# Performance work log

Hardware: AMD Instinct MI355X
Metric: run time of the kernel (lower is better)

## Reference

```python
import jax, jax.numpy as jnp
import numpy as np

DIM = 2048
N_HEADS = 16
HEAD_DIM = 128

def setup_inputs() -> dict:
    key = jax.random.key(0)
    ks = jax.random.split(key, 7)
    B, S = 4, 2048
    x = jax.random.normal(ks[0], (B, S, DIM), dtype=jnp.float32)
    cos = jax.random.uniform(ks[1], (S, HEAD_DIM // 2), dtype=jnp.float32)
    sin = jax.random.uniform(ks[2], (S, HEAD_DIM // 2), dtype=jnp.float32)
    scale = 1.0 / np.sqrt(DIM)
    wq = jax.random.normal(ks[3], (DIM, N_HEADS * HEAD_DIM), dtype=jnp.float32) * scale
    wk = jax.random.normal(ks[4], (DIM, N_HEADS * HEAD_DIM), dtype=jnp.float32) * scale
    wv = jax.random.normal(ks[5], (DIM, N_HEADS * HEAD_DIM), dtype=jnp.float32) * scale
    wo = jax.random.normal(ks[6], (N_HEADS * HEAD_DIM, DIM), dtype=jnp.float32) * scale
    return {"x": x, "cos": cos, "sin": sin, "wq": wq, "wk": wk, "wv": wv, "wo": wo}

def _apply_rope(x, cos, sin):
    # x: [B, H, S, D]; cos/sin: [S, D//2]
    d = x.shape[-1] // 2
    x1, x2 = x[..., :d], x[..., d:]
    c = cos[None, None, :x.shape[2], :d]
    s = sin[None, None, :x.shape[2], :d]
    return jnp.concatenate([x1 * c - x2 * s, x2 * c + x1 * s], axis=-1)

def reference(x, cos, sin, wq, wk, wv, wo):
    B, S, _ = x.shape
    q = (x @ wq).reshape(B, S, N_HEADS, HEAD_DIM).transpose(0, 2, 1, 3)
    k = (x @ wk).reshape(B, S, N_HEADS, HEAD_DIM).transpose(0, 2, 1, 3)
    v = (x @ wv).reshape(B, S, N_HEADS, HEAD_DIM).transpose(0, 2, 1, 3)
    q = _apply_rope(q, cos, sin)
    k = _apply_rope(k, cos, sin)
    scale = 1.0 / jnp.sqrt(jnp.asarray(HEAD_DIM, dtype=x.dtype))
    scores = jnp.einsum('bhqd,bhkd->bhqk', q, k) * scale  # [B,H,S,S]
    causal = jnp.tril(jnp.ones((S, S), dtype=bool))
    scores = jnp.where(causal[None, None], scores, jnp.asarray(-jnp.inf, dtype=scores.dtype))
    attn = jax.nn.softmax(scores, axis=-1)
    out = jnp.einsum('bhqk,bhkd->bhqd', attn, v)
    out = out.transpose(0, 2, 1, 3).reshape(B, S, N_HEADS * HEAD_DIM)
    return out @ wo
```

## Files before the change

### kernel.cpp

```cpp
#include <hip/hip_runtime.h>
#include <cstdint>
#include <cstddef>

#define DIM 2048
#define NHEADS 16
#define HD 128
#define BATCH 4
#define SEQ 2048
#define MROWS (BATCH*SEQ)
#define NT 32
#define TSZ (256*64)

typedef __attribute__((ext_vector_type(4))) float  f32x4;
typedef __attribute__((ext_vector_type(4))) float  float4v;
typedef __attribute__((ext_vector_type(8))) short  short8;
typedef __attribute__((ext_vector_type(4))) short  short4v;
typedef __attribute__((ext_vector_type(4))) unsigned uint4v;
typedef __attribute__((ext_vector_type(8))) __bf16 bf16x8;

#define QSCALE 0.1275173772f

__device__ __forceinline__ unsigned f2bfbits(float f) {
  unsigned u = __builtin_bit_cast(unsigned, f);
  return (u + 0x7FFFu + ((u >> 16) & 1u)) >> 16;
}
__device__ __forceinline__ short f2bf(float f) { return (short)f2bfbits(f); }
__device__ __forceinline__ float bf2f(short s) {
  unsigned u = ((unsigned)(unsigned short)s) << 16;
  return __builtin_bit_cast(float, u);
}
__device__ __forceinline__ unsigned cvtpk_bf16(float lo, float hi) {
  unsigned r;
  asm("v_cvt_pk_bf16_f32 %0, %1, %2" : "=v"(r) : "v"(lo), "v"(hi));
  return r;
}
__device__ __forceinline__ f32x4 mfma16(short8 a, short8 b, f32x4 c) {
  return __builtin_amdgcn_mfma_f32_16x16x32_bf16(
      __builtin_bit_cast(bf16x8, a), __builtin_bit_cast(bf16x8, b), c, 0, 0, 0);
}
__device__ __forceinline__ void gload16(const short* g, short* l) {
  __builtin_amdgcn_global_load_lds(
      (const __attribute__((address_space(1))) unsigned int*)g,
      (__attribute__((address_space(3))) unsigned int*)l, 16, 0, 0);
}

__global__ __launch_bounds__(256) void k_convert_x(const float* __restrict__ x,
                                                   short* __restrict__ xb) {
  size_t i = ((size_t)blockIdx.x * 256 + threadIdx.x) * 8;
  float4v a = *(const float4v*)(x + i);
  float4v b = *(const float4v*)(x + i + 4);
  short8 o;
  o[0] = f2bf(a[0]); o[1] = f2bf(a[1]); o[2] = f2bf(a[2]); o[3] = f2bf(a[3]);
  o[4] = f2bf(b[0]); o[5] = f2bf(b[1]); o[6] = f2bf(b[2]); o[7] = f2bf(b[3]);
  *(short8*)(xb + i) = o;
}

__global__ __launch_bounds__(256) void k_transpose_w(
    const float* __restrict__ w0, const float* __restrict__ w1,
    const float* __restrict__ w2, const float* __restrict__ w3,
    short* __restrict__ o0, short* __restrict__ o1,
    short* __restrict__ o2, short* __restrict__ o3) {
  const float* w; short* o;
  switch (blockIdx.z) {
    case 0: w = w0; o = o0; break;
    case 1: w = w1; o = o1; break;
    case 2: w = w2; o = o2; break;
    default: w = w3; o = o3; break;
  }
  __shared__ float tile[32][33];
  int tx = threadIdx.x, ty = threadIdx.y;
  int kb = blockIdx.y * 32, nb = blockIdx.x * 32;
#pragma unroll
  for (int i = 0; i < 4; ++i)
    tile[ty + 8 * i][tx] = w[(size_t)(kb + ty + 8 * i) * DIM + nb + tx];
  __syncthreads();
#pragma unroll
  for (int i = 0; i < 4; ++i)
    o[(size_t)(nb + ty + 8 * i) * DIM + kb + tx] = f2bf(tile[tx][ty + 8 * i]);
}

template<int MODE>
__global__ __launch_bounds__(512, 2) void k_gemm256(const short* __restrict__ A,
                                                    const short* __restrict__ BtAll,
                                                    const float* __restrict__ cosg,
                                                    const float* __restrict__ sing,
                                                    short* __restrict__ Qp,
                                                    short* __restrict__ Kp,
                                                    short* __restrict__ Vp,
                                                    float* __restrict__ Of) {
  __shared__ short As[2 * TSZ];
  __shared__ short Bs[2 * TSZ];
  const int t = threadIdx.x;
  const int lane = t & 63, wid = t >> 6;
  const int wm = wid >> 2, wn = wid & 3;
  const int gi = lane >> 4, li = lane & 15;
  const int stg = (wid ^ (wid >> 2)) & 1;
  const int id = blockIdx.x;
  const int wg = MODE == 0 ? ((id & 7) * 96 + (id >> 3)) : ((id & 7) * 32 + (id >> 3));
  const int bm = wg & 31, bn = wg >> 5;
  const int m0 = bm * 256;
  const int which = MODE == 0 ? (bn >> 3) : 0;
  const int n0 = MODE == 0 ? ((bn & 7) * 256) : (bn * 256);
  const short* Bg = BtAll + (size_t)which * DIM * DIM;
  const short* Ag = A;

  const int lrow = lane >> 3;
  const int lcol = ((lane & 7) ^ lrow) * 8;
  const int hh = wn >> 1, hf = wn & 1;

  auto bcol = [&](int j) {
    if (MODE == 0) return hh * 128 + (j >> 1) * 64 + hf * 32 + (j & 1) * 16;
    return wn * 64 + j * 16;
  };

  f32x4 acc[8][4];
#pragma unroll
  for (int i = 0; i < 8; ++i)
#pragma unroll
    for (int j = 0; j < 4; ++j) acc[i][j] = (f32x4){0.f, 0.f, 0.f, 0.f};

#define STAGE_TILE(tt, buf)                                                       \
  {                                                                               \
    const int kk0 = (tt) * 64;                                                    \
    short* asd = As + (buf) * TSZ;                                                \
    short* bsd = Bs + (buf) * TSZ;                                                \
    _Pragma("unroll")                                                             \
    for (int ii = 0; ii < 4; ++ii) {                                              \
      int rb = ii * 64 + wid * 8;                                                 \
      gload16(Ag + (size_t)(m0 + rb + lrow) * DIM + kk0 + lcol, asd + rb * 64);   \
      gload16(Bg + (size_t)(n0 + rb + lrow) * DIM + kk0 + lcol, bsd + rb * 64);   \
    }                                                                             \
  }

  STAGE_TILE(0, 0)
  STAGE_TILE(1, 1)

  for (int tt = 0; tt < NT; ++tt) {
    if (tt < NT - 1) asm volatile("s_waitcnt vmcnt(8)" ::: "memory");
    else             asm volatile("s_waitcnt vmcnt(0)" ::: "memory");
    __builtin_amdgcn_s_barrier();
    const short* Asb = As + (tt & 1) * TSZ;
    const short* Bsb = Bs + (tt & 1) * TSZ;

#pragma unroll 1
    for (int ph = 0; ph < 2; ++ph) {
      const int ks = ph ^ stg;
      short8 av[8], bv[4];
      const int sw = (((ks << 2) | gi) ^ (li & 7)) * 8;
#pragma unroll
      for (int i = 0; i < 8; ++i)
        av[i] = *(const short8*)&Asb[(wm * 128 + i * 16 + li) * 64 + sw];
#pragma unroll
      for (int j = 0; j < 4; ++j)
        bv[j] = *(const short8*)&Bsb[(bcol(j) + li) * 64 + sw];
      __builtin_amdgcn_s_setprio(1);
#pragma unroll
      for (int i = 0; i < 8; ++i)
#pragma unroll
        for (int j = 0; j < 4; ++j)
          acc[i][j] = mfma16(av[i], bv[j], acc[i][j]);
      __builtin_amdgcn_s_setprio(0);
    }
    __builtin_amdgcn_s_barrier();
    if (tt + 2 < NT) STAGE_TILE(tt + 2, tt & 1)
  }
#undef STAGE_TILE

  if (MODE == 1) {
#pragma unroll
    for (int i = 0; i < 8; ++i)
#pragma unroll
      for (int j = 0; j < 4; ++j)
#pragma unroll
        for (int r = 0; r < 4; ++r) {
          int gm = m0 + wm * 128 + i * 16 + gi * 4 + r;
          int gn = n0 + wn * 64 + j * 16 + li;
          Of[(size_t)gm * DIM + gn] = acc[i][j][r];
        }
    return;
  }
  const int h = 2 * (bn & 7) + hh;
  if (which == 2) {
#pragma unroll
    for (int i = 0; i < 8; ++i)
#pragma unroll
      for (int j = 0; j < 4; ++j) {
        int gm0 = m0 + wm * 128 + i * 16 + gi * 4;
        int b = gm0 >> 11, s0 = gm0 & 2047;
        int d = (j >> 1) * 64 + hf * 32 + (j & 1) * 16 + li;
        short4v pk;
#pragma unroll
        for (int r = 0; r < 4; ++r) pk[r] = f2bf(acc[i][j][r]);
        *(short4v*)&Vp[((size_t)(b * NHEADS + h) * HD + d) * SEQ + s0] = pk;
      }
  } else {
    short* O = which ? Kp : Qp;
    const float qs = which ? 1.0f : QSCALE;
#pragma unroll
    for (int i = 0; i < 8; ++i)
#pragma unroll
      for (int j = 0; j < 2; ++j) {
        int dlo = hf * 32 + j * 16 + li;
#pragma unroll
        for (int r = 0; r < 4; ++r) {
          int gm = m0 + wm * 128 + i * 16 + gi * 4 + r;
          int b = gm >> 11, s = gm & 2047;
          float c = cosg[s * 64 + dlo], sn = sing[s * 64 + dlo];
          float a = acc[i][j][r], bb = acc[i][j + 2][r];
          size_t base = ((size_t)(b * NHEADS + h) * SEQ + s) * HD;
          O[base + dlo]      = f2bf((a * c - bb * sn) * qs);
          O[base + dlo + 64] = f2bf((bb * c + a * sn) * qs);
        }
      }
  }
}

__global__ __launch_bounds__(512) void k_flash(const short* __restrict__ Qg,
                                               const short* __restrict__ Kg,
                                               const short* __restrict__ Vg,
                                               short* __restrict__ Og) {
  __shared__ short Kl[2 * 64 * 128];
  __shared__ short Vl[2 * 128 * 64];
  const int t = threadIdx.x, lane = t & 63, wid = t >> 6;
  const int gi = lane >> 4, li = lane & 15;
  const int id = blockIdx.x;
  const int ip = 15 - (id >> 6);
  const int bh = id & 63;
  const int q0 = ip * 128;
  const short* Qb = Qg + (size_t)bh * SEQ * HD;
  const short* Kb = Kg + (size_t)bh * SEQ * HD;
  const short* Vb = Vg + (size_t)bh * HD * SEQ;
  const int mrow = q0 + wid * 16 + li;
  const int nt = 2 * ip + 2;

  short8 qb[4];
#pragma unroll
  for (int kk = 0; kk < 4; ++kk)
    qb[kk] = *(const short8*)(Qb + (size_t)mrow * HD + kk * 32 + 8 * gi);

  f32x4 o[8];
#pragma unroll
  for (int d = 0; d < 8; ++d) o[d] = (f32x4){0.f, 0.f, 0.f, 0.f};
  float mx = -1e30f, lsum = 0.f;
  const int srcA = li | ((lane & 16) << 1);
  const int srcB = srcA + 16;
  const bool hig = (lane & 32) != 0;

#define FSTAGE(tt, buf)                                                           \
  {                                                                               \
    const int kk0 = (tt) * 64;                                                    \
    short* kl = Kl + (buf) * 8192;                                                \
    short* vl = Vl + (buf) * 8192;                                                \
    _Pragma("unroll")                                                             \
    for (int u = 0; u < 2; ++u) {                                                 \
      int w = wid * 2 + u;                                                        \
      { int row = w * 4 + (lane >> 4); int sl = (lane & 15) ^ (row & 15);         \
        gload16(Kb + (size_t)(kk0 + row) * HD + sl * 8, kl + w * 512); }          \
      { int row = w * 8 + (lane >> 3); int sl = (lane & 7) ^ (row & 7);           \
        gload16(Vb + (size_t)row * SEQ + kk0 + sl * 8, vl + w * 512); }           \
    }                                                                             \
  }

  FSTAGE(0, 0)

  for (int tt = 0; tt < nt; ++tt) {
    const int k0 = tt * 64;
    if (tt + 1 < nt) {
      FSTAGE(tt + 1, (tt + 1) & 1)
      asm volatile("s_waitcnt vmcnt(4)" ::: "memory");
    } else {
      asm volatile("s_waitcnt vmcnt(0)" ::: "memory");
    }
    __builtin_amdgcn_s_barrier();
    const short* Kc = Kl + (tt & 1) * 8192;
    const short* Vc = Vl + (tt & 1) * 8192;

    f32x4 sacc[4];
#pragma unroll
    for (int af = 0; af < 4; ++af) sacc[af] = (f32x4){0.f, 0.f, 0.f, 0.f};
    __builtin_amdgcn_s_setprio(1);
#pragma unroll
    for (int kk = 0; kk < 4; ++kk)
#pragma unroll
      for (int af = 0; af < 4; ++af) {
        short8 kf = *(const short8*)&Kc[(16 * af + li) * 128 + (((kk << 2) | gi) ^ li) * 8];
        sacc[af] = mfma16(kf, qb[kk], sacc[af]);
      }
    __builtin_amdgcn_s_setprio(0);

    float p[4][4];
    float pmax = -1e30f;
    const bool mask = (k0 + 63 > mrow);
#pragma unroll
    for (int af = 0; af < 4; ++af)
#pragma unroll
      for (int r = 0; r < 4; ++r) {
        float v = sacc[af][r];
        if (mask && (k0 + 16 * af + 4 * gi + r > mrow)) v = -1e30f;
        p[af][r] = v;
        pmax = fmaxf(pmax, v);
      }
    pmax = fmaxf(pmax, __shfl_xor(pmax, 16));
    pmax = fmaxf(pmax, __shfl_xor(pmax, 32));
    if (!__all(pmax <= mx + 11.54f)) {
      float mnew = fmaxf(mx, pmax);
      float alpha = __builtin_amdgcn_exp2f(mx - mnew);
      lsum *= alpha;
      mx = mnew;
#pragma unroll
      for (int d = 0; d < 8; ++d) o[d] *= alpha;
    }
    float psum = 0.f;
#pragma unroll
    for (int af = 0; af < 4; ++af)
#pragma unroll
      for (int r = 0; r < 4; ++r) {
        float e = __builtin_amdgcn_exp2f(p[af][r] - mx);
        p[af][r] = e;
        psum += e;
      }
    psum += __shfl_xor(psum, 16);
    psum += __shfl_xor(psum, 32);
    lsum += psum;

    unsigned plo[4], phi[4];
#pragma unroll
    for (int af = 0; af < 4; ++af) {
      plo[af] = cvtpk_bf16(p[af][0], p[af][1]);
      phi[af] = cvtpk_bf16(p[af][2], p[af][3]);
    }
#pragma unroll
    for (int kk2 = 0; kk2 < 2; ++kk2) {
      unsigned aAlo = (unsigned)__shfl((int)plo[2 * kk2], srcA);
      unsigned aAhi = (unsigned)__shfl((int)phi[2 * kk2], srcA);
      unsigned aBlo = (unsigned)__shfl((int)plo[2 * kk2 + 1], srcA);
      unsigned aBhi = (unsigned)__shfl((int)phi[2 * kk2 + 1], srcA);
      unsigned bAlo = (unsigned)__shfl((int)plo[2 * kk2], srcB);
      unsigned bAhi = (unsigned)__shfl((int)phi[2 * kk2], srcB);
      unsigned bBlo = (unsigned)__shfl((int)plo[2 * kk2 + 1], srcB);
      unsigned bBhi = (unsigned)__shfl((int)phi[2 * kk2 + 1], srcB);
      uint4v dws;
      dws[0] = hig ? aBlo : aAlo;
      dws[1] = hig ? aBhi : aAhi;
      dws[2] = hig ? bBlo : bAlo;
      dws[3] = hig ? bBhi : bAhi;
      short8 pbf = __builtin_bit_cast(short8, dws);
      __builtin_amdgcn_s_setprio(1);
#pragma unroll
      for (int d = 0; d < 8; ++d) {
        short8 vf = *(const short8*)&Vc[(16 * d + li) * 64 + ((((kk2 << 2) | gi)) ^ (li & 7)) * 8];
        o[d] = mfma16(vf, pbf, o[d]);
      }
      __builtin_amdgcn_s_setprio(0);
    }
    __builtin_amdgcn_s_barrier();
  }
#undef FSTAGE

  const float inv = 1.0f / lsum;
  const int b = bh >> 4, h = bh & 15;
  const size_t obase = ((size_t)b * SEQ + mrow) * DIM + h * HD;
#pragma unroll
  for (int d = 0; d < 8; ++d) {
    short4v st;
#pragma unroll
    for (int r = 0; r < 4; ++r) st[r] = f2bf(o[d][r] * inv);
    *(short4v*)&Og[obase + d * 16 + 4 * gi] = st;
  }
}

extern "C" void kernel_launch(void* const* d_in, const int* in_sizes, int n_in,
                              void* d_out, int out_size, void* d_ws, size_t ws_size,
                              hipStream_t stream) {
  (void)in_sizes; (void)n_in; (void)out_size;
  const float* x    = (const float*)d_in[0];
  const float* cosg = (const float*)d_in[1];
  const float* sing = (const float*)d_in[2];
  const float* wq   = (const float*)d_in[3];
  const float* wk   = (const float*)d_in[4];
  const float* wv   = (const float*)d_in[5];
  const float* wo   = (const float*)d_in[6];

  const size_t SZ = (size_t)MROWS * DIM * 2;
  char* ws = (char*)d_ws;
  short* xb  = (short*)ws;
  short* wqT = (short*)(ws + SZ);
  short* wkT = wqT + (size_t)DIM * DIM;
  short* wvT = wkT + (size_t)DIM * DIM;
  short* woT = wvT + (size_t)DIM * DIM;
  short *Qp, *Kp, *Vp;
  if (ws_size >= 5 * SZ) {
    Qp = (short*)(ws + 2 * SZ);
    Kp = (short*)(ws + 3 * SZ);
    Vp = (short*)(ws + 4 * SZ);
  } else {
    Qp = (short*)d_out;
    Kp = (short*)d_out + SZ / 2;
    Vp = (short*)(ws + 2 * SZ);
  }
  short* Ob = xb;

  k_convert_x<<<8192, 256, 0, stream>>>(x, xb);
  k_transpose_w<<<dim3(64, 64, 4), dim3(32, 8), 0, stream>>>(wq, wk, wv, wo,
                                                             wqT, wkT, wvT, woT);
  k_gemm256<0><<<768, 512, 0, stream>>>(xb, wqT, cosg, sing, Qp, Kp, Vp, nullptr);
  k_flash<<<1024, 512, 0, stream>>>(Qp, Kp, Vp, Ob);
  k_gemm256<1><<<256, 512, 0, stream>>>(Ob, woT, nullptr, nullptr,
                                        nullptr, nullptr, nullptr, (float*)d_out);
}
```

Measured before the change: 434.7 us.

## Interleave half-tile global loads with MFMA phases in the 256x256 GEMM

```diff
diff --git a/kernel.cpp b/kernel.cpp
--- a/kernel.cpp
+++ b/kernel.cpp
@@ -80,7 +80,7 @@
 }
 
 template<int MODE>
-__global__ __launch_bounds__(512, 2) void k_gemm256(const short* __restrict__ A,
+__global__ __launch_bounds__(512, 1) void k_gemm256(const short* __restrict__ A,
                                                     const short* __restrict__ BtAll,
                                                     const float* __restrict__ cosg,
                                                     const float* __restrict__ sing,
@@ -94,7 +94,6 @@
   const int lane = t & 63, wid = t >> 6;
   const int wm = wid >> 2, wn = wid & 3;
   const int gi = lane >> 4, li = lane & 15;
-  const int stg = (wid ^ (wid >> 2)) & 1;
   const int id = blockIdx.x;
   const int wg = MODE == 0 ? ((id & 7) * 96 + (id >> 3)) : ((id & 7) * 32 + (id >> 3));
   const int bm = wg & 31, bn = wg >> 5;
@@ -113,58 +112,89 @@
     return wn * 64 + j * 16;
   };
 
+  auto stageA = [&](int h, int tile) {
+    const int kk0 = tile * 64;
+    short* d = As + (tile & 1) * TSZ;
+#pragma unroll
+    for (int u = 0; u < 2; ++u) {
+      int rb = h * 128 + u * 64 + wid * 8;
+      gload16(Ag + (size_t)(m0 + rb + lrow) * DIM + kk0 + lcol, d + rb * 64);
+    }
+  };
+  auto stageB = [&](int h, int tile) {
+    const int kk0 = tile * 64;
+    short* d = Bs + (tile & 1) * TSZ;
+#pragma unroll
+    for (int u = 0; u < 2; ++u) {
+      int rb = h * 128 + u * 64 + wid * 8;
+      gload16(Bg + (size_t)(n0 + rb + lrow) * DIM + kk0 + lcol, d + rb * 64);
+    }
+  };
+
   f32x4 acc[8][4];
 #pragma unroll
   for (int i = 0; i < 8; ++i)
 #pragma unroll
     for (int j = 0; j < 4; ++j) acc[i][j] = (f32x4){0.f, 0.f, 0.f, 0.f};
 
-#define STAGE_TILE(tt, buf)                                                       \
-  {                                                                               \
-    const int kk0 = (tt) * 64;                                                    \
-    short* asd = As + (buf) * TSZ;                                                \
-    short* bsd = Bs + (buf) * TSZ;                                                \
+#define READ_AV(IH, KS)                                                           \
+  { const int sw = ((((KS) << 2) | gi) ^ (li & 7)) * 8;                           \
     _Pragma("unroll")                                                             \
-    for (int ii = 0; ii < 4; ++ii) {                                              \
-      int rb = ii * 64 + wid * 8;                                                 \
-      gload16(Ag + (size_t)(m0 + rb + lrow) * DIM + kk0 + lcol, asd + rb * 64);   \
-      gload16(Bg + (size_t)(n0 + rb + lrow) * DIM + kk0 + lcol, bsd + rb * 64);   \
-    }                                                                             \
-  }
-
-  STAGE_TILE(0, 0)
-  STAGE_TILE(1, 1)
+    for (int i = 0; i < 4; ++i)                                                   \
+      av[i] = *(const short8*)&Ab[(wm * 128 + ((IH) * 4 + i) * 16 + li) * 64 + sw]; }
+#define READ_BV(DST, KS)                                                          \
+  { const int sw = ((((KS) << 2) | gi) ^ (li & 7)) * 8;                           \
+    _Pragma("unroll")                                                             \
+    for (int j = 0; j < 4; ++j)                                                   \
+      DST[j] = *(const short8*)&Bb[(bcol(j) + li) * 64 + sw]; }
+#define PHASE_MFMA(IH, BV)                                                        \
+  __builtin_amdgcn_s_barrier();                                                   \
+  __builtin_amdgcn_s_setprio(1);                                                  \
+  _Pragma("unroll")                                                               \
+  for (int i = 0; i < 4; ++i)                                                     \
+    _Pragma("unroll")                                                             \
+    for (int j = 0; j < 4; ++j)                                                   \
+      acc[(IH) * 4 + i][j] = mfma16(av[i], BV[j], acc[(IH) * 4 + i][j]);          \
+  __builtin_amdgcn_s_setprio(0);
+
+  stageB(0, 0); stageB(1, 0);
+  stageA(0, 0); stageA(1, 0);
+  stageB(0, 1); stageB(1, 1);
+  asm volatile("s_waitcnt vmcnt(4)" ::: "memory");
+  __builtin_amdgcn_s_barrier();
 
   for (int tt = 0; tt < NT; ++tt) {
-    if (tt < NT - 1) asm volatile("s_waitcnt vmcnt(8)" ::: "memory");
+    const short* Ab = As + (tt & 1) * TSZ;
+    const short* Bb = Bs + (tt & 1) * TSZ;
+    short8 av[4], bv0[4], bv1[4];
+
+    READ_AV(0, 0)
+    READ_BV(bv0, 0)
+    if (tt + 1 < NT) stageA(0, tt + 1);
+    PHASE_MFMA(0, bv0)
+    __builtin_amdgcn_s_barrier();
+
+    READ_AV(0, 1)
+    READ_BV(bv1, 1)
+    if (tt + 1 < NT) stageA(1, tt + 1);
+    PHASE_MFMA(0, bv1)
+    __builtin_amdgcn_s_barrier();
+
+    READ_AV(1, 0)
+    if (tt + 2 < NT) stageB(0, tt + 2);
+    PHASE_MFMA(1, bv0)
+    __builtin_amdgcn_s_barrier();
+
+    READ_AV(1, 1)
+    if (tt + 2 < NT) stageB(1, tt + 2);
+    PHASE_MFMA(1, bv1)
+    if (tt + 2 < NT) asm volatile("s_waitcnt vmcnt(4)" ::: "memory");
     else             asm volatile("s_waitcnt vmcnt(0)" ::: "memory");
     __builtin_amdgcn_s_barrier();
-    const short* Asb = As + (tt & 1) * TSZ;
-    const short* Bsb = Bs + (tt & 1) * TSZ;
-
-#pragma unroll 1
-    for (int ph = 0; ph < 2; ++ph) {
-      const int ks = ph ^ stg;
-      short8 av[8], bv[4];
-      const int sw = (((ks << 2) | gi) ^ (li & 7)) * 8;
-#pragma unroll
-      for (int i = 0; i < 8; ++i)
-        av[i] = *(const short8*)&Asb[(wm * 128 + i * 16 + li) * 64 + sw];
-#pragma unroll
-      for (int j = 0; j < 4; ++j)
-        bv[j] = *(const short8*)&Bsb[(bcol(j) + li) * 64 + sw];
-      __builtin_amdgcn_s_setprio(1);
-#pragma unroll
-      for (int i = 0; i < 8; ++i)
-#pragma unroll
-        for (int j = 0; j < 4; ++j)
-          acc[i][j] = mfma16(av[i], bv[j], acc[i][j]);
-      __builtin_amdgcn_s_setprio(0);
-    }
-    __builtin_amdgcn_s_barrier();
-    if (tt + 2 < NT) STAGE_TILE(tt + 2, tt & 1)
-  }
-#undef STAGE_TILE
+  }
+#undef READ_AV
+#undef READ_BV
+#undef PHASE_MFMA
 
   if (MODE == 1) {
 #pragma unroll
@@ -225,7 +255,7 @@
   const int gi = lane >> 4, li = lane & 15;
   const int id = blockIdx.x;
   const int ip = 15 - (id >> 6);
-  const int bh = id & 63;
+  const int bh = (id & 7) * 8 + ((id >> 3) & 7);
   const int q0 = ip * 128;
   const short* Qb = Qg + (size_t)bh * SEQ * HD;
   const short* Kb = Kg + (size_t)bh * SEQ * HD;
```

Result: faster. 413.5 us (-4.9%).
